# Kernel tuning notes

Measured on AMD Instinct MI355X. Metric: run time of the kernel, lower is better.

Reference implementation:

```python
import jax, jax.numpy as jnp
import numpy as np

B, S, D, H = 4, 2048, 1024, 16
HD = D // H

def setup_inputs() -> dict:
    key = jax.random.key(0)
    ks = jax.random.split(key, 5)
    x = jax.random.normal(ks[0], (B, S, D), dtype=jnp.float32)
    # learned params (torch Linear: y = x @ W.T + b)
    s1 = 1.0 / np.sqrt(D)
    Wqkv = jax.random.uniform(ks[1], (3 * D, D), jnp.float32, -s1, s1)
    bqkv = jax.random.uniform(ks[2], (3 * D,), jnp.float32, -s1, s1)
    Wproj = jax.random.uniform(ks[3], (D, D), jnp.float32, -s1, s1)
    bproj = jax.random.uniform(ks[4], (D,), jnp.float32, -s1, s1)
    # causal mask, broadcast over batch and heads; 0 -> masked
    mask = jnp.tril(jnp.ones((S, S), jnp.int32))[None, None]
    return {"x": x, "Wqkv": Wqkv, "bqkv": bqkv, "Wproj": Wproj, "bproj": bproj, "mask": mask}

def reference(x, Wqkv, bqkv, Wproj, bproj, mask):
    b, s, d = x.shape
    qkv = x @ Wqkv.T + bqkv                      # [B,S,3D]
    qkv = qkv.reshape(b, s, 3, H, HD).transpose(2, 0, 3, 1, 4)  # [3,B,H,S,HD]
    q, k, v = qkv[0], qkv[1], qkv[2]
    scores = jnp.einsum('bhqd,bhkd->bhqk', q, k) / np.sqrt(HD).astype(np.float32)
    scores = jnp.where(mask == 0, -jnp.inf, scores)
    attn = jax.nn.softmax(scores, axis=-1)
    ctx = jnp.einsum('bhqk,bhkd->bhqd', attn, v)  # [B,H,S,HD]
    ctx = ctx.transpose(0, 2, 1, 3).reshape(b, s, d)
    return ctx @ Wproj.T + bproj
```

## Files before the change

kernel.cpp:

```cpp
#include <hip/hip_runtime.h>
#include <stdint.h>

typedef __bf16 bf16;
typedef __bf16 bf16x4 __attribute__((ext_vector_type(4)));
typedef __bf16 bf16x8 __attribute__((ext_vector_type(8)));
typedef float f32x4 __attribute__((ext_vector_type(4)));
typedef short short4v __attribute__((ext_vector_type(4)));

#define NB 4
#define NS 2048
#define ND 1024
#define NH 16
#define NHD 64
#define QSCALE 0.1803368801111204f
#define FMAX   8.0f
#define CPITCH 136

typedef const __attribute__((address_space(1))) unsigned GU;
typedef __attribute__((address_space(3))) unsigned LU;

__device__ __forceinline__ bf16x8 load8f(const float* p) {
    float4 a = *(const float4*)p;
    float4 b = *(const float4*)(p + 4);
    bf16x8 r;
    r[0] = (bf16)a.x; r[1] = (bf16)a.y; r[2] = (bf16)a.z; r[3] = (bf16)a.w;
    r[4] = (bf16)b.x; r[5] = (bf16)b.y; r[6] = (bf16)b.z; r[7] = (bf16)b.w;
    return r;
}
__device__ __forceinline__ void store8(bf16* p, bf16x8 v) { *(bf16x8*)p = v; }
__device__ __forceinline__ void store8(float* p, bf16x8 v) {
    float4 a; a.x = (float)v[0]; a.y = (float)v[1]; a.z = (float)v[2]; a.w = (float)v[3];
    float4 b; b.x = (float)v[4]; b.y = (float)v[5]; b.z = (float)v[6]; b.w = (float)v[7];
    *(float4*)p = a; *(float4*)(p + 4) = b;
}

__device__ __forceinline__ f32x4 mfma16(bf16x4 a, bf16x4 b, f32x4 c) {
#ifdef __HIP_DEVICE_COMPILE__
#if __has_builtin(__builtin_amdgcn_mfma_f32_16x16x16bf16_1k)
    return __builtin_amdgcn_mfma_f32_16x16x16bf16_1k(
        __builtin_bit_cast(short4v, a), __builtin_bit_cast(short4v, b), c, 0, 0, 0);
#else
    f32x4 d;
    asm("v_mfma_f32_16x16x16_bf16 %0, %1, %2, %3"
        : "=v"(d) : "v"(a), "v"(b), "v"(c));
    return d;
#endif
#else
    return c;
#endif
}

__device__ __forceinline__ int sw(int row, int col) {
    return row * 72 + (col ^ (((row >> 2) & 3) * 16));
}

__global__ __launch_bounds__(256)
void convert_kernel(const float* __restrict__ s0, bf16* __restrict__ d0, int n0,
                    const float* __restrict__ s1, bf16* __restrict__ d1, int n1,
                    const float* __restrict__ s2, bf16* __restrict__ d2, int n2)
{
    int idx = (blockIdx.x * 256 + threadIdx.x) * 8;
    const float* s; bf16* d;
    if (idx < n0)              { s = s0 + idx;  d = d0 + idx; }
    else if ((idx -= n0) < n1) { s = s1 + idx;  d = d1 + idx; }
    else if ((idx -= n1) < n2) { s = s2 + idx;  d = d2 + idx; }
    else return;
    *(bf16x8*)d = load8f(s);
}

template<typename TO, int MODE>
__device__ __forceinline__ void gemm_epilogue(
    f32x4 (&acc)[4][4], bf16* Ls, const float* __restrict__ bias,
    TO* __restrict__ O0, bf16* __restrict__ O1, bf16* __restrict__ O2,
    int N, int m0, int n0, int tid)
{
    const int lane = tid & 63;
    const int w = tid >> 6, wm = w >> 1, wn = w & 1;
    const int lr = lane & 15, quad = lane >> 4;
    const int cls = (MODE == 0) ? (n0 >> 10) : 1;

    if (MODE == 0 && cls == 2) {
#pragma unroll
        for (int im = 0; im < 4; ++im) {
            int rowb = wm * 64 + im * 16 + quad * 4;
#pragma unroll
            for (int in = 0; in < 4; ++in) {
                int col = wn * 64 + in * 16 + lr;
                float bv = bias[n0 + col];
                bf16x4 pv;
#pragma unroll
                for (int r = 0; r < 4; ++r) pv[r] = (bf16)(acc[im][in][r] + bv);
                *(bf16x4*)&Ls[col * CPITCH + rowb] = pv;
            }
        }
        __syncthreads();
        const int b = m0 >> 11, s0 = m0 & 2047;
#pragma unroll
        for (int p = 0; p < 8; ++p) {
            int idx = tid + 256 * p;
            int col = idx & 127, mg = idx >> 7;
            bf16x8 v8 = *(const bf16x8*)&Ls[col * CPITCH + mg * 8];
            int ncol = n0 + col;
            int h = (ncol >> 6) & 15, hd = ncol & 63;
            *(bf16x8*)&((bf16*)O0)[((size_t)(b * NH + h) * NHD + hd) * NS + s0 + mg * 8] = v8;
        }
    } else {
#pragma unroll
        for (int im = 0; im < 4; ++im) {
            int rowb = wm * 64 + im * 16 + quad * 4;
#pragma unroll
            for (int in = 0; in < 4; ++in) {
                int col = wn * 64 + in * 16 + lr;
                float bv = bias[n0 + col];
#pragma unroll
                for (int r = 0; r < 4; ++r) {
                    float v = acc[im][in][r] + bv;
                    if (MODE == 0 && cls == 0) v *= QSCALE;
                    Ls[(rowb + r) * CPITCH + col] = (bf16)v;
                }
            }
        }
        __syncthreads();
#pragma unroll
        for (int p = 0; p < 8; ++p) {
            int idx = tid + 256 * p;
            int row = idx >> 4, colg = (idx & 15) * 8;
            bf16x8 v8 = *(const bf16x8*)&Ls[row * CPITCH + colg];
            if (MODE == 0) {
                int ncol = n0 + colg;
                int h = (ncol >> 6) & 15, hd = ncol & 63;
                int m = m0 + row, b = m >> 11, s = m & 2047;
                bf16* dst = (cls == 0) ? O1 : O2;
                *(bf16x8*)&dst[((size_t)(b * NH + h) * NS + s) * NHD + hd] = v8;
            } else {
                store8(&O0[(size_t)(m0 + row) * N + n0 + colg], v8);
            }
        }
    }
}

template<typename TO, int MODE>
__global__ __launch_bounds__(256, 3)
void gemm_bt(const bf16* __restrict__ Xp, const bf16* __restrict__ Wp,
             const float* __restrict__ bias, TO* __restrict__ O0,
             bf16* __restrict__ O1, bf16* __restrict__ O2, int N, int K)
{
    __shared__ union {
        struct { bf16 Ah[128 * 32]; bf16 Bh[128 * 32]; } s;
        bf16 C[128 * CPITCH];
    } u;
    const int tid  = threadIdx.x;
    const int lane = tid & 63;
    const int w    = tid >> 6;
    const int wm   = w >> 1, wn = w & 1;
    const int lr   = lane & 15, quad = lane >> 4;
    const int m0   = blockIdx.y * 128;
    const int n0   = blockIdx.x * 128;

    const int srow = w * 32 + (lane >> 2);
    const int scol = (lane & 3) * 8;
    const bf16* gA = Xp + (size_t)(m0 + srow) * K + scol;
    const bf16* gB = Wp + (size_t)(n0 + srow) * K + scol;

    f32x4 acc[4][4] = {};

    for (int k0 = 0; k0 < K; k0 += 32) {
#pragma unroll
        for (int c = 0; c < 2; ++c) {
            __builtin_amdgcn_global_load_lds((GU*)(gA + (size_t)c * 16 * K + k0),
                                             (LU*)&u.s.Ah[(w * 32 + c * 16) * 32], 16, 0, 0);
            __builtin_amdgcn_global_load_lds((GU*)(gB + (size_t)c * 16 * K + k0),
                                             (LU*)&u.s.Bh[(w * 32 + c * 16) * 32], 16, 0, 0);
        }
        __syncthreads();

        bf16x8 af[4], bfr[4];
#pragma unroll
        for (int im = 0; im < 4; ++im)
            af[im] = *(const bf16x8*)(&u.s.Ah[(wm * 64 + im * 16 + lr) * 32 + quad * 8]);
#pragma unroll
        for (int in = 0; in < 4; ++in)
            bfr[in] = *(const bf16x8*)(&u.s.Bh[(wn * 64 + in * 16 + lr) * 32 + quad * 8]);
#pragma unroll
        for (int im = 0; im < 4; ++im)
#pragma unroll
            for (int in = 0; in < 4; ++in)
                acc[im][in] = __builtin_amdgcn_mfma_f32_16x16x32_bf16(
                    af[im], bfr[in], acc[im][in], 0, 0, 0);
        __syncthreads();
    }

    gemm_epilogue<TO, MODE>(acc, u.C, bias, O0, O1, O2, N, m0, n0, tid);
}

__global__ __launch_bounds__(256, 5)
void attn_kernel(const bf16* __restrict__ Q, const bf16* __restrict__ K,
                 const bf16* __restrict__ Vt_g, bf16* __restrict__ ctx)
{
    const int jt = 31 - (blockIdx.x >> 6);
    const int bh = blockIdx.x & 63;
    const int b  = bh >> 4, h = bh & 15;
    const int q0 = jt * 64;
    const bf16* Qp = Q + (size_t)bh * NS * NHD;
    const bf16* Kp = K + (size_t)bh * NS * NHD;
    const bf16* Vp = Vt_g + (size_t)bh * NHD * NS;

    __shared__ bf16 Qh[64 * 72];
    __shared__ bf16 Kh[64 * 72];
    __shared__ bf16 Vh[64 * 72];

    const int tid  = threadIdx.x;
    const int lane = tid & 63;
    const int w    = tid >> 6;
    const int lr   = lane & 15, quad = lane >> 4;

#pragma unroll
    for (int i = 0; i < 2; ++i) {
        int c = tid + 256 * i;
        int row = c >> 3, ch = c & 7;
        *(bf16x8*)(&Qh[sw(row, ch * 8)]) =
            *(const bf16x8*)(Qp + (size_t)(q0 + row) * NHD + ch * 8);
    }

    const int qrow = q0 + w * 16 + lr;
    float l_part = 0.f;
    f32x4 acco[4] = {};

    const int nkt = jt + 1;
    for (int kt = 0; kt < nkt; ++kt) {
        __syncthreads();
#pragma unroll
        for (int i = 0; i < 2; ++i) {
            int c = tid + 256 * i;
            int row = c >> 3, ch = c & 7;
            *(bf16x8*)(&Kh[sw(row, ch * 8)]) =
                *(const bf16x8*)(Kp + (size_t)(kt * 64 + row) * NHD + ch * 8);
            *(bf16x8*)(&Vh[sw(row, ch * 8)]) =
                *(const bf16x8*)(Vp + (size_t)row * NS + kt * 64 + ch * 8);
        }
        __syncthreads();

        f32x4 sacc[4] = {};
#pragma unroll
        for (int ks = 0; ks < 2; ++ks) {
            bf16x8 bq = *(const bf16x8*)(&Qh[sw(w * 16 + lr, ks * 32 + quad * 8)]);
#pragma unroll
            for (int kn = 0; kn < 4; ++kn) {
                bf16x8 ak = *(const bf16x8*)(&Kh[sw(kn * 16 + lr, ks * 32 + quad * 8)]);
                sacc[kn] = __builtin_amdgcn_mfma_f32_16x16x32_bf16(ak, bq, sacc[kn], 0, 0, 0);
            }
        }

        const bool diag = (kt == jt);
        bf16x4 pf[4];
#pragma unroll
        for (int kn = 0; kn < 4; ++kn) {
#pragma unroll
            for (int r = 0; r < 4; ++r) {
                float x = sacc[kn][r];
                if (diag) {
                    int kcol = kt * 64 + kn * 16 + quad * 4 + r;
                    x = (kcol <= qrow) ? x : -INFINITY;
                }
                float p = __builtin_amdgcn_exp2f(x - FMAX);
                l_part += p;
                pf[kn][r] = (bf16)p;
            }
        }

#pragma unroll
        for (int kn = 0; kn < 4; ++kn) {
#pragma unroll
            for (int jn = 0; jn < 4; ++jn) {
                bf16x4 av = *(const bf16x4*)(&Vh[sw(jn * 16 + lr, kn * 16 + quad * 4)]);
                acco[jn] = mfma16(av, pf[kn], acco[jn]);
            }
        }
    }

    float l = l_part;
    l += __shfl_xor(l, 16);
    l += __shfl_xor(l, 32);
    float rinv = 1.0f / l;

    __syncthreads();
#pragma unroll
    for (int jn = 0; jn < 4; ++jn) {
        bf16x4 pv;
#pragma unroll
        for (int r = 0; r < 4; ++r) pv[r] = (bf16)(acco[jn][r] * rinv);
        *(bf16x4*)&Qh[(w * 16 + lr) * 72 + jn * 16 + quad * 4] = pv;
    }
    __syncthreads();
#pragma unroll
    for (int p = 0; p < 2; ++p) {
        int idx = tid + 256 * p;
        int row = idx >> 3, colg = (idx & 7) * 8;
        bf16x8 v8 = *(const bf16x8*)&Qh[row * 72 + colg];
        *(bf16x8*)&ctx[((size_t)(b * NS) + q0 + row) * ND + h * NHD + colg] = v8;
    }
}

extern "C" void kernel_launch(void* const* d_in, const int* in_sizes, int n_in,
                              void* d_out, int out_size, void* d_ws, size_t ws_size,
                              hipStream_t stream) {
    const float* x     = (const float*)d_in[0];
    const float* Wqkv  = (const float*)d_in[1];
    const float* bqkv  = (const float*)d_in[2];
    const float* Wproj = (const float*)d_in[3];
    const float* bproj = (const float*)d_in[4];
    float* out = (float*)d_out;

    const size_t per = (size_t)NB * NH * NS * NHD;
    bf16* q_ws = (bf16*)d_ws;
    bf16* k_ws = q_ws + per;
    bf16* v_ws = k_ws + per;
    bf16* x_bf = v_ws + per;
    bf16* c_ws = x_bf;
    bf16* wq_bf = x_bf + per;
    bf16* wp_bf = wq_bf + (size_t)3 * ND * ND;

    const int n0 = NB * NS * ND;
    const int n1 = 3 * ND * ND;
    const int n2 = ND * ND;
    convert_kernel<<<(n0 + n1 + n2) / (256 * 8), 256, 0, stream>>>(
        x, x_bf, n0, Wqkv, wq_bf, n1, Wproj, wp_bf, n2);

    dim3 gq(3 * ND / 128, NB * NS / 128);
    gemm_bt<bf16, 0><<<gq, 256, 0, stream>>>(
        x_bf, wq_bf, bqkv, v_ws, q_ws, k_ws, 3 * ND, ND);

    attn_kernel<<<dim3(NB * NH * 32), 256, 0, stream>>>(q_ws, k_ws, v_ws, c_ws);

    dim3 gp(ND / 128, NB * NS / 128);
    gemm_bt<float, 1><<<gp, 256, 0, stream>>>(
        c_ws, wp_bf, bproj, out, nullptr, nullptr, ND, ND);
}
```

Measured before the change: 277.1 us.

## Enlarge attention query tile to 128 rows so each wave handles two row groups

```diff
diff --git a/kernel.cpp b/kernel.cpp
--- a/kernel.cpp
+++ b/kernel.cpp
@@ -193,21 +193,22 @@
     gemm_epilogue<TO, MODE>(acc, u.C, bias, O0, O1, O2, N, m0, n0, tid);
 }
 
-__global__ __launch_bounds__(256, 5)
+__global__ __launch_bounds__(256, 3)
 void attn_kernel(const bf16* __restrict__ Q, const bf16* __restrict__ K,
                  const bf16* __restrict__ Vt_g, bf16* __restrict__ ctx)
 {
-    const int jt = 31 - (blockIdx.x >> 6);
+    const int jt = 15 - (blockIdx.x >> 6);
     const int bh = blockIdx.x & 63;
     const int b  = bh >> 4, h = bh & 15;
-    const int q0 = jt * 64;
+    const int q0 = jt * 128;
     const bf16* Qp = Q + (size_t)bh * NS * NHD;
     const bf16* Kp = K + (size_t)bh * NS * NHD;
     const bf16* Vp = Vt_g + (size_t)bh * NHD * NS;
 
-    __shared__ bf16 Qh[64 * 72];
-    __shared__ bf16 Kh[64 * 72];
-    __shared__ bf16 Vh[64 * 72];
+    __shared__ union {
+        struct { bf16 Kh[64 * 72]; bf16 Vh[64 * 72]; } s;
+        bf16 QO[128 * 72];
+    } u;
 
     const int tid  = threadIdx.x;
     const int lane = tid & 63;
@@ -215,88 +216,109 @@
     const int lr   = lane & 15, quad = lane >> 4;
 
 #pragma unroll
-    for (int i = 0; i < 2; ++i) {
+    for (int i = 0; i < 4; ++i) {
         int c = tid + 256 * i;
         int row = c >> 3, ch = c & 7;
-        *(bf16x8*)(&Qh[sw(row, ch * 8)]) =
+        *(bf16x8*)(&u.QO[sw(row, ch * 8)]) =
             *(const bf16x8*)(Qp + (size_t)(q0 + row) * NHD + ch * 8);
     }
-
-    const int qrow = q0 + w * 16 + lr;
-    float l_part = 0.f;
-    f32x4 acco[4] = {};
-
-    const int nkt = jt + 1;
+    __syncthreads();
+
+    bf16x8 qf[2][2];
+#pragma unroll
+    for (int qg = 0; qg < 2; ++qg)
+#pragma unroll
+        for (int ks = 0; ks < 2; ++ks)
+            qf[qg][ks] = *(const bf16x8*)(&u.QO[sw(w * 32 + qg * 16 + lr, ks * 32 + quad * 8)]);
+
+    float l_part[2] = {0.f, 0.f};
+    f32x4 acco[2][4] = {};
+
+    const int wq0 = q0 + w * 32;
+    const int nkt = 2 * jt + 2;
     for (int kt = 0; kt < nkt; ++kt) {
         __syncthreads();
 #pragma unroll
         for (int i = 0; i < 2; ++i) {
             int c = tid + 256 * i;
             int row = c >> 3, ch = c & 7;
-            *(bf16x8*)(&Kh[sw(row, ch * 8)]) =
+            *(bf16x8*)(&u.s.Kh[sw(row, ch * 8)]) =
                 *(const bf16x8*)(Kp + (size_t)(kt * 64 + row) * NHD + ch * 8);
-            *(bf16x8*)(&Vh[sw(row, ch * 8)]) =
+            *(bf16x8*)(&u.s.Vh[sw(row, ch * 8)]) =
                 *(const bf16x8*)(Vp + (size_t)row * NS + kt * 64 + ch * 8);
         }
         __syncthreads();
 
-        f32x4 sacc[4] = {};
+        if (kt * 64 > wq0 + 31) continue;
+
+        f32x4 sacc[2][4] = {};
 #pragma unroll
         for (int ks = 0; ks < 2; ++ks) {
-            bf16x8 bq = *(const bf16x8*)(&Qh[sw(w * 16 + lr, ks * 32 + quad * 8)]);
 #pragma unroll
             for (int kn = 0; kn < 4; ++kn) {
-                bf16x8 ak = *(const bf16x8*)(&Kh[sw(kn * 16 + lr, ks * 32 + quad * 8)]);
-                sacc[kn] = __builtin_amdgcn_mfma_f32_16x16x32_bf16(ak, bq, sacc[kn], 0, 0, 0);
-            }
-        }
-
-        const bool diag = (kt == jt);
-        bf16x4 pf[4];
+                bf16x8 ak = *(const bf16x8*)(&u.s.Kh[sw(kn * 16 + lr, ks * 32 + quad * 8)]);
+                sacc[0][kn] = __builtin_amdgcn_mfma_f32_16x16x32_bf16(ak, qf[0][ks], sacc[0][kn], 0, 0, 0);
+                sacc[1][kn] = __builtin_amdgcn_mfma_f32_16x16x32_bf16(ak, qf[1][ks], sacc[1][kn], 0, 0, 0);
+            }
+        }
+
+        const bool diag = (kt * 64 + 63 > wq0);
+        bf16x4 pf[2][4];
+#pragma unroll
+        for (int qg = 0; qg < 2; ++qg) {
+            const int qrow = wq0 + qg * 16 + lr;
+#pragma unroll
+            for (int kn = 0; kn < 4; ++kn) {
+#pragma unroll
+                for (int r = 0; r < 4; ++r) {
+                    float x = sacc[qg][kn][r];
+                    if (diag) {
+                        int kcol = kt * 64 + kn * 16 + quad * 4 + r;
+                        x = (kcol <= qrow) ? x : -INFINITY;
+                    }
+                    float p = __builtin_amdgcn_exp2f(x - FMAX);
+                    l_part[qg] += p;
+                    pf[qg][kn][r] = (bf16)p;
+                }
+            }
+        }
+
 #pragma unroll
         for (int kn = 0; kn < 4; ++kn) {
 #pragma unroll
-            for (int r = 0; r < 4; ++r) {
-                float x = sacc[kn][r];
-                if (diag) {
-                    int kcol = kt * 64 + kn * 16 + quad * 4 + r;
-                    x = (kcol <= qrow) ? x : -INFINITY;
-                }
-                float p = __builtin_amdgcn_exp2f(x - FMAX);
-                l_part += p;
-                pf[kn][r] = (bf16)p;
-            }
-        }
-
-#pragma unroll
-        for (int kn = 0; kn < 4; ++kn) {
-#pragma unroll
             for (int jn = 0; jn < 4; ++jn) {
-                bf16x4 av = *(const bf16x4*)(&Vh[sw(jn * 16 + lr, kn * 16 + quad * 4)]);
-                acco[jn] = mfma16(av, pf[kn], acco[jn]);
-            }
-        }
-    }
-
-    float l = l_part;
-    l += __shfl_xor(l, 16);
-    l += __shfl_xor(l, 32);
-    float rinv = 1.0f / l;
+                bf16x4 av = *(const bf16x4*)(&u.s.Vh[sw(jn * 16 + lr, kn * 16 + quad * 4)]);
+                acco[0][jn] = mfma16(av, pf[0][kn], acco[0][jn]);
+                acco[1][jn] = mfma16(av, pf[1][kn], acco[1][jn]);
+            }
+        }
+    }
+
+    float rinv[2];
+#pragma unroll
+    for (int qg = 0; qg < 2; ++qg) {
+        float l = l_part[qg];
+        l += __shfl_xor(l, 16);
+        l += __shfl_xor(l, 32);
+        rinv[qg] = 1.0f / l;
+    }
 
     __syncthreads();
 #pragma unroll
-    for (int jn = 0; jn < 4; ++jn) {
-        bf16x4 pv;
-#pragma unroll
-        for (int r = 0; r < 4; ++r) pv[r] = (bf16)(acco[jn][r] * rinv);
-        *(bf16x4*)&Qh[(w * 16 + lr) * 72 + jn * 16 + quad * 4] = pv;
-    }
+    for (int qg = 0; qg < 2; ++qg)
+#pragma unroll
+        for (int jn = 0; jn < 4; ++jn) {
+            bf16x4 pv;
+#pragma unroll
+            for (int r = 0; r < 4; ++r) pv[r] = (bf16)(acco[qg][jn][r] * rinv[qg]);
+            *(bf16x4*)&u.QO[(w * 32 + qg * 16 + lr) * 72 + jn * 16 + quad * 4] = pv;
+        }
     __syncthreads();
 #pragma unroll
-    for (int p = 0; p < 2; ++p) {
+    for (int p = 0; p < 4; ++p) {
         int idx = tid + 256 * p;
         int row = idx >> 3, colg = (idx & 7) * 8;
-        bf16x8 v8 = *(const bf16x8*)&Qh[row * 72 + colg];
+        bf16x8 v8 = *(const bf16x8*)&u.QO[row * 72 + colg];
         *(bf16x8*)&ctx[((size_t)(b * NS) + q0 + row) * ND + h * NHD + colg] = v8;
     }
 }
@@ -330,7 +352,7 @@
     gemm_bt<bf16, 0><<<gq, 256, 0, stream>>>(
         x_bf, wq_bf, bqkv, v_ws, q_ws, k_ws, 3 * ND, ND);
 
-    attn_kernel<<<dim3(NB * NH * 32), 256, 0, stream>>>(q_ws, k_ws, v_ws, c_ws);
+    attn_kernel<<<dim3(NB * NH * 16), 256, 0, stream>>>(q_ws, k_ws, v_ws, c_ws);
 
     dim3 gp(ND / 128, NB * NS / 128);
     gemm_bt<float, 1><<<gp, 256, 0, stream>>>(
```

Result: slower. 291.5 us (+5.2%).
